# Performance work log

Measured on AMD Instinct MI355X. Metric: run time of the kernel, lower is better.

The kernel has to match this reference:

```python
import jax, jax.numpy as jnp
import numpy as np

N = 262144
IN_FEATURES = 63
LATENT = 64
NUM_CLUSTERS = 256


def setup_inputs() -> dict:
    key = jax.random.key(0)
    k1, k2, k3, k4 = jax.random.split(key, 4)
    X = jax.random.normal(k1, (N, IN_FEATURES + LATENT), dtype=jnp.float32)
    cluster_ids = jax.random.randint(k2, (N,), 0, NUM_CLUSTERS, dtype=jnp.int32)
    W_pos = jax.random.normal(k3, (3 * NUM_CLUSTERS, IN_FEATURES), dtype=jnp.float32) * 0.1
    W_feat = jax.random.normal(k4, (3 * NUM_CLUSTERS, LATENT), dtype=jnp.float32) * 0.1
    return {"X": X, "cluster_ids": cluster_ids, "W_pos": W_pos, "W_feat": W_feat}


def reference(X, cluster_ids, W_pos, W_feat):
    # Dense projection to all clusters: [N, 3*num_clusters]
    X_pos = X[:, :-LATENT]          # [N, in_features]
    X_lat = X[:, -LATENT:]          # [N, latent_size]
    rgb_clusters = X_pos @ W_pos.T + X_lat @ W_feat.T
    # Per-row gather of the 3 columns belonging to this row's cluster.
    cols = 3 * cluster_ids[:, None] + jnp.arange(3, dtype=cluster_ids.dtype)[None, :]  # [N, 3]
    rgb = jnp.take_along_axis(rgb_clusters, cols, axis=1)  # [N, 3]
    return rgb
```

## Files before the change

kernel.cpp:

```cpp
#include <hip/hip_runtime.h>


constexpr int ROWW = 127;
constexpr int NC   = 256;

template <int CTRL, int RMASK, int BMASK>
__device__ __forceinline__ float dpp_add(float x) {
    int t = __builtin_amdgcn_update_dpp(0, __builtin_bit_cast(int, x),
                                        CTRL, RMASK, BMASK, false);
    return x + __builtin_bit_cast(float, t);
}

__device__ __forceinline__ float row_sum(float x) {
    x = dpp_add<0xB1,  0xF, 0xF>(x);
    x = dpp_add<0x4E,  0xF, 0xF>(x);
    x = dpp_add<0x114, 0xF, 0xE>(x);
    x = dpp_add<0x118, 0xF, 0xC>(x);
    return x;
}

__device__ __forceinline__ float wave_sum63(float x) {
    x = row_sum(x);
    x = dpp_add<0x142, 0xA, 0xF>(x);
    x = dpp_add<0x143, 0xC, 0xF>(x);
    return x;
}

__device__ __forceinline__ unsigned f2bf(float f) {
    unsigned u = __builtin_bit_cast(unsigned, f);
    return (u + 0x7fffu + ((u >> 16) & 1u)) >> 16;
}
__device__ __forceinline__ float blo(unsigned u) {
    return __builtin_bit_cast(float, u << 16);
}
__device__ __forceinline__ float bhi(unsigned u) {
    return __builtin_bit_cast(float, u & 0xffff0000u);
}


__device__ __forceinline__ float wval(const float* Wp, const float* Wf,
                                      int r, int f) {
    if (f < 63)  return Wp[(size_t)r * 63 + f];
    if (f == 63) return Wf[(size_t)r * 64];
    if (f < 127) return Wf[(size_t)r * 64 + (f - 63)];
    return 0.0f;
}

__global__ __launch_bounds__(256) void k_pack(const float* __restrict__ Wp,
                                              const float* __restrict__ Wf,
                                              uint4* __restrict__ Wt) {
    const int c   = blockIdx.x * 16 + (threadIdx.x >> 4);
    const int l16 = threadIdx.x & 15;
    #pragma unroll
    for (int j = 0; j < 3; ++j) {
        const int r = 3 * c + j;
        uint4 q;
        q.x = f2bf(wval(Wp, Wf, r, l16))       | (f2bf(wval(Wp, Wf, r, 16 + l16))  << 16);
        q.y = f2bf(wval(Wp, Wf, r, 32 + l16))  | (f2bf(wval(Wp, Wf, r, 48 + l16))  << 16);
        q.z = f2bf(wval(Wp, Wf, r, 64 + l16))  | (f2bf(wval(Wp, Wf, r, 80 + l16))  << 16);
        q.w = f2bf(wval(Wp, Wf, r, 96 + l16))  | (f2bf(wval(Wp, Wf, r, 112 + l16)) << 16);
        Wt[(size_t)(c * 3 + j) * 16 + l16] = q;
    }
}

__device__ __forceinline__ float dot8(const uint4& q,
                                      float x0, float x1, float x2, float x3,
                                      float x4, float x5, float x6, float x7) {
    return fmaf(x0, blo(q.x), x1 * bhi(q.x)) + fmaf(x2, blo(q.y), x3 * bhi(q.y))
         + fmaf(x4, blo(q.z), x5 * bhi(q.z)) + fmaf(x6, blo(q.w), x7 * bhi(q.w));
}


__global__ __launch_bounds__(256, 8) void k_main_pipe(
    const float* __restrict__ X,
    const int*   __restrict__ cid,
    const uint4* __restrict__ Wt,
    float*       __restrict__ out,
    int npts)
{
    const int lane = threadIdx.x & 63;
    const int l16  = lane & 15;
    const int qr   = lane >> 4;
    const bool leader = (l16 == 15);
    const int o7   = leader ? 126 : 112 + l16;
    const int wid  = (blockIdx.x * blockDim.x + threadIdx.x) >> 6;
    const int nW   = (gridDim.x * blockDim.x) >> 6;
    const int step = nW * 4;
    const int last = npts - 1;
    const int niter = npts / step;

    int p = wid * 4 + qr;

    int c = cid[p];
    const float* xr0 = X + (size_t)p * ROWW;
    float x0 = xr0[l16],      x1 = xr0[16 + l16];
    float x2 = xr0[32 + l16], x3 = xr0[48 + l16];
    float x4 = xr0[64 + l16], x5 = xr0[80 + l16];
    float x6 = xr0[96 + l16], x7 = xr0[o7];

    for (int t = 0; t < niter; ++t) {
        const uint4* wb = Wt + (size_t)c * 48 + l16;
        const uint4 q0 = wb[0];
        const uint4 q1 = wb[16];
        const uint4 q2 = wb[32];
        __builtin_amdgcn_sched_barrier(0);

        int pn = p + step;
        if (pn > last) pn = last;
        const int cn = cid[pn];
        const float* yr = X + (size_t)pn * ROWW;
        const float y0 = yr[l16],      y1 = yr[16 + l16];
        const float y2 = yr[32 + l16], y3 = yr[48 + l16];
        const float y4 = yr[64 + l16], y5 = yr[80 + l16];
        const float y6 = yr[96 + l16], y7 = yr[o7];
        __builtin_amdgcn_sched_barrier(0);

        float a0 = dot8(q0, x0, x1, x2, x3, x4, x5, x6, x7);
        float a1 = dot8(q1, x0, x1, x2, x3, x4, x5, x6, x7);
        float a2 = dot8(q2, x0, x1, x2, x3, x4, x5, x6, x7);

        a0 = row_sum(a0);
        a1 = row_sum(a1);
        a2 = row_sum(a2);

        if (leader) {
            float* o = out + 3 * (size_t)p;
            o[0] = a0; o[1] = a1; o[2] = a2;
        }

        p += step; c = cn;
        x0 = y0; x1 = y1; x2 = y2; x3 = y3;
        x4 = y4; x5 = y5; x6 = y6; x7 = y7;
    }
}


__global__ __launch_bounds__(256, 8) void k_main(
    const float* __restrict__ X,
    const int*   __restrict__ cid,
    const uint4* __restrict__ Wt,
    float*       __restrict__ out,
    int npts)
{
    const int lane = threadIdx.x & 63;
    const int l16  = lane & 15;
    const int qr   = lane >> 4;
    const bool leader = (l16 == 15);
    const int o7   = leader ? 126 : 112 + l16;
    const int wid  = (blockIdx.x * blockDim.x + threadIdx.x) >> 6;
    const int nW   = (gridDim.x * blockDim.x) >> 6;
    const int step = nW * 4;
    const int last = npts - 1;
    const int niter = (npts + step - 1) / step;

    int p = wid * 4 + qr;
    int c = cid[min(p, last)];

    for (int t = 0; t < niter; ++t) {
        const int pc = min(p, last);
        const float* xr = X + (size_t)pc * ROWW;
        const float x0 = xr[l16];
        const float x1 = xr[16 + l16];
        const float x2 = xr[32 + l16];
        const float x3 = xr[48 + l16];
        const float x4 = xr[64 + l16];
        const float x5 = xr[80 + l16];
        const float x6 = xr[96 + l16];
        const float x7 = xr[o7];

        const int pn = p + step;
        const int cn = cid[min(pn, last)];

        const uint4* wb = Wt + (size_t)c * 48 + l16;
        const uint4 q0 = wb[0];
        const uint4 q1 = wb[16];
        const uint4 q2 = wb[32];

        float a0 = dot8(q0, x0, x1, x2, x3, x4, x5, x6, x7);
        float a1 = dot8(q1, x0, x1, x2, x3, x4, x5, x6, x7);
        float a2 = dot8(q2, x0, x1, x2, x3, x4, x5, x6, x7);

        a0 = row_sum(a0);
        a1 = row_sum(a1);
        a2 = row_sum(a2);

        if (leader && p < npts) {
            float* o = out + 3 * (size_t)p;
            o[0] = a0; o[1] = a1; o[2] = a2;
        }

        p = pn; c = cn;
    }
}


__global__ __launch_bounds__(256, 8) void lad_fallback(
    const float* __restrict__ X, const int* __restrict__ cid,
    const float* __restrict__ Wp, const float* __restrict__ Wf,
    float* __restrict__ out, int npts)
{
    const int lane  = threadIdx.x & 63;
    const int wid   = (blockIdx.x * blockDim.x + threadIdx.x) >> 6;
    const int nW    = (gridDim.x * blockDim.x) >> 6;
    const int lanec = (lane < 63) ? lane : 62;
    const bool l63  = (lane == 63);

    for (int n = wid; n < npts; n += 2 * nW) {
        const int n2 = n + nW;
        const bool has2 = (n2 < npts);

        const float* x0 = X + (size_t)n * ROWW;
        float xa0 = x0[lane];
        float xb0 = x0[63 + lane];
        int   c0  = __builtin_amdgcn_readfirstlane(cid[n]);

        float xa1 = 0.0f, xb1 = 0.0f;
        int   c1  = 0;
        if (has2) {
            const float* x1 = X + (size_t)n2 * ROWW;
            xa1 = x1[lane];
            xb1 = x1[63 + lane];
            c1  = __builtin_amdgcn_readfirstlane(cid[n2]);
        }
        if (l63) { xa0 = 0.0f; xa1 = 0.0f; }

        const float* wp0 = Wp + (size_t)(3 * c0) * 63;
        const float* wf0 = Wf + (size_t)(3 * c0) * 64;
        const float* wp1 = Wp + (size_t)(3 * c1) * 63;
        const float* wf1 = Wf + (size_t)(3 * c1) * 64;

        float a00 = fmaf(xa0, wp0[lanec],       xb0 * wf0[lane]);
        float a01 = fmaf(xa0, wp0[63 + lanec],  xb0 * wf0[64 + lane]);
        float a02 = fmaf(xa0, wp0[126 + lanec], xb0 * wf0[128 + lane]);
        float a10 = fmaf(xa1, wp1[lanec],       xb1 * wf1[lane]);
        float a11 = fmaf(xa1, wp1[63 + lanec],  xb1 * wf1[64 + lane]);
        float a12 = fmaf(xa1, wp1[126 + lanec], xb1 * wf1[128 + lane]);

        a00 = wave_sum63(a00); a01 = wave_sum63(a01); a02 = wave_sum63(a02);
        a10 = wave_sum63(a10); a11 = wave_sum63(a11); a12 = wave_sum63(a12);

        if (l63) {
            float* o0 = out + 3 * (size_t)n;
            o0[0] = a00; o0[1] = a01; o0[2] = a02;
            if (has2) {
                float* o1 = out + 3 * (size_t)n2;
                o1[0] = a10; o1[1] = a11; o1[2] = a12;
            }
        }
    }
}

extern "C" void kernel_launch(void* const* d_in, const int* in_sizes, int n_in,
                              void* d_out, int out_size, void* d_ws, size_t ws_size,
                              hipStream_t stream) {
    const float* X   = (const float*)d_in[0];
    const int*   cid = (const int*)d_in[1];
    const float* Wp  = (const float*)d_in[2];
    const float* Wf  = (const float*)d_in[3];
    float* out = (float*)d_out;
    const int npts = in_sizes[1];

    const size_t wt_bytes = (size_t)NC * 3 * 16 * sizeof(uint4);
    if (ws_size < wt_bytes) {
        dim3 grid(2048), block(256);
        hipLaunchKernelGGL(lad_fallback, grid, block, 0, stream,
                           X, cid, Wp, Wf, out, npts);
        return;
    }

    uint4* Wt = (uint4*)d_ws;
    hipLaunchKernelGGL(k_pack, dim3(NC / 16), dim3(256), 0, stream, Wp, Wf, Wt);

    const int nW = (2048 * 256) >> 6;
    const int step = nW * 4;
    if (npts % step == 0) {
        hipLaunchKernelGGL(k_main_pipe, dim3(2048), dim3(256), 0, stream,
                           X, cid, Wt, out, npts);
    } else {
        hipLaunchKernelGGL(k_main, dim3(2048), dim3(256), 0, stream,
                           X, cid, Wt, out, npts);
    }
}
```

Before: 32.69 us.

## Vectorize X row loads into two 16-byte loads per lane with contiguous weight packing

Reorders the packed bf16 weight layout so each lane owns 8 contiguous features, letting every lane fetch its slice of an X row with two 4-wide vector loads instead of eight scalar loads. The final 126-element row edge is handled by clamping the second load and shifting components. Output stores are spread over three lanes rather than three serial stores from one leader lane. Rows of 127 floats are not 16-byte aligned, so the vector loads may be unaligned, and the row_sum reduction must still yield correct totals on the storing lanes.

```diff
diff --git a/kernel.cpp b/kernel.cpp
--- a/kernel.cpp
+++ b/kernel.cpp
@@ -3,6 +3,8 @@
 
 constexpr int ROWW = 127;
 constexpr int NC   = 256;
+
+typedef float f32x4v __attribute__((ext_vector_type(4), aligned(4)));
 
 template <int CTRL, int RMASK, int BMASK>
 __device__ __forceinline__ float dpp_add(float x) {
@@ -37,7 +39,6 @@
     return __builtin_bit_cast(float, u & 0xffff0000u);
 }
 
-
 __device__ __forceinline__ float wval(const float* Wp, const float* Wf,
                                       int r, int f) {
     if (f < 63)  return Wp[(size_t)r * 63 + f];
@@ -46,19 +47,21 @@
     return 0.0f;
 }
 
+
 __global__ __launch_bounds__(256) void k_pack(const float* __restrict__ Wp,
                                               const float* __restrict__ Wf,
                                               uint4* __restrict__ Wt) {
     const int c   = blockIdx.x * 16 + (threadIdx.x >> 4);
     const int l16 = threadIdx.x & 15;
+    const int f   = 8 * l16;
     #pragma unroll
     for (int j = 0; j < 3; ++j) {
         const int r = 3 * c + j;
         uint4 q;
-        q.x = f2bf(wval(Wp, Wf, r, l16))       | (f2bf(wval(Wp, Wf, r, 16 + l16))  << 16);
-        q.y = f2bf(wval(Wp, Wf, r, 32 + l16))  | (f2bf(wval(Wp, Wf, r, 48 + l16))  << 16);
-        q.z = f2bf(wval(Wp, Wf, r, 64 + l16))  | (f2bf(wval(Wp, Wf, r, 80 + l16))  << 16);
-        q.w = f2bf(wval(Wp, Wf, r, 96 + l16))  | (f2bf(wval(Wp, Wf, r, 112 + l16)) << 16);
+        q.x = f2bf(wval(Wp, Wf, r, f + 0)) | (f2bf(wval(Wp, Wf, r, f + 1)) << 16);
+        q.y = f2bf(wval(Wp, Wf, r, f + 2)) | (f2bf(wval(Wp, Wf, r, f + 3)) << 16);
+        q.z = f2bf(wval(Wp, Wf, r, f + 4)) | (f2bf(wval(Wp, Wf, r, f + 5)) << 16);
+        q.w = f2bf(wval(Wp, Wf, r, f + 6)) | (f2bf(wval(Wp, Wf, r, f + 7)) << 16);
         Wt[(size_t)(c * 3 + j) * 16 + l16] = q;
     }
 }
@@ -81,22 +84,25 @@
     const int lane = threadIdx.x & 63;
     const int l16  = lane & 15;
     const int qr   = lane >> 4;
-    const bool leader = (l16 == 15);
-    const int o7   = leader ? 126 : 112 + l16;
     const int wid  = (blockIdx.x * blockDim.x + threadIdx.x) >> 6;
     const int nW   = (gridDim.x * blockDim.x) >> 6;
     const int step = nW * 4;
     const int last = npts - 1;
     const int niter = npts / step;
+    const size_t T = (size_t)npts * ROWW;
 
     int p = wid * 4 + qr;
 
     int c = cid[p];
-    const float* xr0 = X + (size_t)p * ROWW;
-    float x0 = xr0[l16],      x1 = xr0[16 + l16];
-    float x2 = xr0[32 + l16], x3 = xr0[48 + l16];
-    float x4 = xr0[64 + l16], x5 = xr0[80 + l16];
-    float x6 = xr0[96 + l16], x7 = xr0[o7];
+    f32x4v xv1, xv2;  bool badc;
+    {
+        const size_t e1 = (size_t)p * ROWW + 8 * l16;
+        size_t e2 = e1 + 4;
+        badc = e2 > T - 4;
+        if (badc) e2 = T - 4;
+        xv1 = *(const f32x4v*)(X + e1);
+        xv2 = *(const f32x4v*)(X + e2);
+    }
 
     for (int t = 0; t < niter; ++t) {
         const uint4* wb = Wt + (size_t)c * 48 + l16;
@@ -108,12 +114,22 @@
         int pn = p + step;
         if (pn > last) pn = last;
         const int cn = cid[pn];
-        const float* yr = X + (size_t)pn * ROWW;
-        const float y0 = yr[l16],      y1 = yr[16 + l16];
-        const float y2 = yr[32 + l16], y3 = yr[48 + l16];
-        const float y4 = yr[64 + l16], y5 = yr[80 + l16];
-        const float y6 = yr[96 + l16], y7 = yr[o7];
+        f32x4v yv1, yv2;  bool badn;
+        {
+            const size_t e1 = (size_t)pn * ROWW + 8 * l16;
+            size_t e2 = e1 + 4;
+            badn = e2 > T - 4;
+            if (badn) e2 = T - 4;
+            yv1 = *(const f32x4v*)(X + e1);
+            yv2 = *(const f32x4v*)(X + e2);
+        }
         __builtin_amdgcn_sched_barrier(0);
+
+        const float x0 = xv1.x, x1 = xv1.y, x2 = xv1.z, x3 = xv1.w;
+        const float x4 = badc ? xv2.y : xv2.x;
+        const float x5 = badc ? xv2.z : xv2.y;
+        const float x6 = badc ? xv2.w : xv2.z;
+        const float x7 = xv2.w;
 
         float a0 = dot8(q0, x0, x1, x2, x3, x4, x5, x6, x7);
         float a1 = dot8(q1, x0, x1, x2, x3, x4, x5, x6, x7);
@@ -123,14 +139,12 @@
         a1 = row_sum(a1);
         a2 = row_sum(a2);
 
-        if (leader) {
-            float* o = out + 3 * (size_t)p;
-            o[0] = a0; o[1] = a1; o[2] = a2;
-        }
-
-        p += step; c = cn;
-        x0 = y0; x1 = y1; x2 = y2; x3 = y3;
-        x4 = y4; x5 = y5; x6 = y6; x7 = y7;
+        const float sv = (l16 == 12) ? a0 : (l16 == 13) ? a1 : a2;
+        if (l16 >= 12 && l16 < 15)
+            out[3 * (size_t)p + (l16 - 12)] = sv;
+
+        p = pn; c = cn;
+        xv1 = yv1; xv2 = yv2; badc = badn;
     }
 }
 
@@ -145,28 +159,24 @@
     const int lane = threadIdx.x & 63;
     const int l16  = lane & 15;
     const int qr   = lane >> 4;
-    const bool leader = (l16 == 15);
-    const int o7   = leader ? 126 : 112 + l16;
     const int wid  = (blockIdx.x * blockDim.x + threadIdx.x) >> 6;
     const int nW   = (gridDim.x * blockDim.x) >> 6;
     const int step = nW * 4;
     const int last = npts - 1;
     const int niter = (npts + step - 1) / step;
+    const size_t T = (size_t)npts * ROWW;
 
     int p = wid * 4 + qr;
     int c = cid[min(p, last)];
 
     for (int t = 0; t < niter; ++t) {
         const int pc = min(p, last);
-        const float* xr = X + (size_t)pc * ROWW;
-        const float x0 = xr[l16];
-        const float x1 = xr[16 + l16];
-        const float x2 = xr[32 + l16];
-        const float x3 = xr[48 + l16];
-        const float x4 = xr[64 + l16];
-        const float x5 = xr[80 + l16];
-        const float x6 = xr[96 + l16];
-        const float x7 = xr[o7];
+        const size_t e1 = (size_t)pc * ROWW + 8 * l16;
+        size_t e2 = e1 + 4;
+        const bool bad = e2 > T - 4;
+        if (bad) e2 = T - 4;
+        const f32x4v xv1 = *(const f32x4v*)(X + e1);
+        const f32x4v xv2 = *(const f32x4v*)(X + e2);
 
         const int pn = p + step;
         const int cn = cid[min(pn, last)];
@@ -176,6 +186,12 @@
         const uint4 q1 = wb[16];
         const uint4 q2 = wb[32];
 
+        const float x0 = xv1.x, x1 = xv1.y, x2 = xv1.z, x3 = xv1.w;
+        const float x4 = bad ? xv2.y : xv2.x;
+        const float x5 = bad ? xv2.z : xv2.y;
+        const float x6 = bad ? xv2.w : xv2.z;
+        const float x7 = xv2.w;
+
         float a0 = dot8(q0, x0, x1, x2, x3, x4, x5, x6, x7);
         float a1 = dot8(q1, x0, x1, x2, x3, x4, x5, x6, x7);
         float a2 = dot8(q2, x0, x1, x2, x3, x4, x5, x6, x7);
@@ -184,10 +200,9 @@
         a1 = row_sum(a1);
         a2 = row_sum(a2);
 
-        if (leader && p < npts) {
-            float* o = out + 3 * (size_t)p;
-            o[0] = a0; o[1] = a1; o[2] = a2;
-        }
+        const float sv = (l16 == 12) ? a0 : (l16 == 13) ? a1 : a2;
+        if (p < npts && l16 >= 12 && l16 < 15)
+            out[3 * (size_t)p + (l16 - 12)] = sv;
 
         p = pn; c = cn;
     }
@@ -273,7 +288,7 @@
 
     const int nW = (2048 * 256) >> 6;
     const int step = nW * 4;
-    if (npts % step == 0) {
+    if (npts % step == 0 && npts > step) {
         hipLaunchKernelGGL(k_main_pipe, dim3(2048), dim3(256), 0, stream,
                            X, cid, Wt, out, npts);
     } else {
```

Result: faster. 31.98 us (-2.2%).
